# Performance work log

Measured on AMD Instinct MI355X. Metric: run time of the kernel, lower is better.

## Reference

```python
import jax, jax.numpy as jnp
import numpy as np

EPS = 1e-10
N_ITERS = 20
TEMP = 1.0


def sinkhorn(log_alpha, temp, n_iters):
    # incomplete Sinkhorn normalization over last two dims
    la = log_alpha / temp
    for _ in range(n_iters):
        la = la - jax.nn.logsumexp(la, axis=-2, keepdims=True)  # column norm
        la = la - jax.nn.logsumexp(la, axis=-1, keepdims=True)  # row norm
    return jnp.exp(la)


def setup_inputs() -> dict:
    key = jax.random.key(0)
    k1, k2, k3 = jax.random.split(key, 3)
    S, B, D, N = 4, 8, 1024, 1024  # samples, batch, feature rows, perm size
    x = jax.random.normal(k1, (B, D, N), dtype=jnp.float32)
    # kaiming_uniform_ default (a=sqrt(5)) -> bound = 1/sqrt(fan_in)
    bound = 1.0 / np.sqrt(N)
    log_alpha = jax.random.uniform(k2, (N, N), jnp.float32, -bound, bound)
    u = jax.random.uniform(k3, (S, B, N, N), jnp.float32)  # uniform draws for gumbel
    return {"x": x, "log_alpha": log_alpha, "u": u}


def reference(x, log_alpha, u):
    # gumbel noise: -log(eps - log(U + eps)) as in sample_gumbel
    gumbel = -jnp.log(EPS - jnp.log(u + EPS))
    log_alpha_noise = log_alpha + gumbel                  # (S,B,N,N)
    soft_perms = sinkhorn(log_alpha_noise, TEMP, N_ITERS)  # (S,B,N,N)
    # x.unsqueeze(0) @ soft_perms -> (S,B,D,N)
    return jnp.einsum('bdn,sbnm->sbdm', x, soft_perms)
```

## Files before the change

### kernel.cpp

```cpp
#include <hip/hip_runtime.h>

#define EPS 1e-10f
#define NITERS 20
#define NN (1024*1024)

typedef __attribute__((ext_vector_type(8))) short bf16x8;
typedef __attribute__((ext_vector_type(4))) float f32x4;

__device__ __forceinline__ unsigned short f2bf(float f) {
  unsigned int x = __builtin_bit_cast(unsigned int, f);
  x += 0x7fffu + ((x >> 16) & 1u);
  return (unsigned short)(x >> 16);
}
__device__ __forceinline__ float bf2f(short s) {
  return __builtin_bit_cast(float, ((unsigned int)(unsigned short)s) << 16);
}

__global__ __launch_bounds__(256) void gumbel_colpass(const float* __restrict__ u,
                                                      const float* __restrict__ la,
                                                      unsigned short* __restrict__ Kb,
                                                      float* __restrict__ pv) {
  int bx = blockIdx.x;
  int sb = bx >> 4, ch = bx & 15;
  int tid = threadIdx.x, l = tid & 63, w = tid >> 6;
  int r0 = ch << 6;
  const float* ub = u + (size_t)sb * NN;
  float colacc[16];
#pragma unroll
  for (int k = 0; k < 16; ++k) colacc[k] = 0.f;

#pragma unroll 1
  for (int p = 0; p < 16; ++p) {
    int row = r0 + (p << 2) + w;
    const float4* u4 = (const float4*)(ub + (size_t)row * 1024 + l * 16);
    const float4* la4 = (const float4*)(la + (size_t)row * 1024 + l * 16);
    float kf[16];
#pragma unroll
    for (int q = 0; q < 4; ++q) {
      float4 uv = u4[q];
      float4 lv = la4[q];
      kf[q*4+0] = expf(lv.x) / (EPS - logf(uv.x + EPS));
      kf[q*4+1] = expf(lv.y) / (EPS - logf(uv.y + EPS));
      kf[q*4+2] = expf(lv.z) / (EPS - logf(uv.z + EPS));
      kf[q*4+3] = expf(lv.w) / (EPS - logf(uv.w + EPS));
    }
    bf16x8 o0, o1;
#pragma unroll
    for (int j = 0; j < 8; ++j) {
      o0[j] = (short)f2bf(kf[j]);
      o1[j] = (short)f2bf(kf[8 + j]);
      colacc[j] += kf[j];
      colacc[8 + j] += kf[8 + j];
    }
    bf16x8* kp = (bf16x8*)(Kb + (size_t)sb * NN + (size_t)row * 1024 + l * 16);
    kp[0] = o0; kp[1] = o1;
  }

  __shared__ float cacc[4][1024];
#pragma unroll
  for (int k = 0; k < 16; ++k) cacc[w][l * 16 + k] = colacc[k];
  __syncthreads();
  float4 s0 = *(float4*)&cacc[0][tid * 4];
  float4 s1 = *(float4*)&cacc[1][tid * 4];
  float4 s2 = *(float4*)&cacc[2][tid * 4];
  float4 s3 = *(float4*)&cacc[3][tid * 4];
  float4 s;
  s.x = s0.x + s1.x + s2.x + s3.x; s.y = s0.y + s1.y + s2.y + s3.y;
  s.z = s0.z + s1.z + s2.z + s3.z; s.w = s0.w + s1.w + s2.w + s3.w;
  ((float4*)pv)[((sb << 4) + ch) * 256 + tid] = s;
}

__global__ __launch_bounds__(256) void sinkhorn_fused(const unsigned short* __restrict__ Kb,
                                                      const float* __restrict__ pv_in,
                                                      float* __restrict__ pv_out) {
  int bx = blockIdx.x;
  int sb = bx >> 4, ch = bx & 15;
  int tid = threadIdx.x, l = tid & 63, w = tid >> 6;
  int r0 = ch << 6;
  __shared__ float smem[4][1024];

  {
    const float4* p4 = (const float4*)pv_in + (sb << 12);
    float4 s = make_float4(0.f, 0.f, 0.f, 0.f);
#pragma unroll
    for (int c = 0; c < 16; ++c) {
      float4 a = p4[c * 256 + tid];
      s.x += a.x; s.y += a.y; s.z += a.z; s.w += a.w;
    }
    float4 v4;
    v4.x = 1.f / s.x; v4.y = 1.f / s.y; v4.z = 1.f / s.z; v4.w = 1.f / s.w;
    *(float4*)&smem[0][tid * 4] = v4;
  }
  __syncthreads();
  float vreg[16];
#pragma unroll
  for (int k = 0; k < 16; ++k) vreg[k] = smem[0][l * 16 + k];
  __syncthreads();

  const unsigned short* Ks = Kb + (size_t)sb * NN;
  float colacc[16];
#pragma unroll
  for (int k = 0; k < 16; ++k) colacc[k] = 0.f;

#pragma unroll 2
  for (int p = 0; p < 16; ++p) {
    int row = r0 + (p << 2) + w;
    const bf16x8* kp = (const bf16x8*)(Ks + (size_t)row * 1024 + l * 16);
    bf16x8 k0 = kp[0], k1 = kp[1];
    float kf[16];
#pragma unroll
    for (int j = 0; j < 8; ++j) { kf[j] = bf2f(k0[j]); kf[8 + j] = bf2f(k1[j]); }
    float dot = 0.f;
#pragma unroll
    for (int k = 0; k < 16; ++k) dot += kf[k] * vreg[k];
#pragma unroll
    for (int m = 1; m < 64; m <<= 1) dot += __shfl_xor(dot, m, 64);
    float ui = 1.0f / dot;
#pragma unroll
    for (int k = 0; k < 16; ++k) colacc[k] += kf[k] * ui;
  }

#pragma unroll
  for (int k = 0; k < 16; ++k) smem[w][l * 16 + k] = colacc[k];
  __syncthreads();
  float4 s0 = *(float4*)&smem[0][tid * 4];
  float4 s1 = *(float4*)&smem[1][tid * 4];
  float4 s2 = *(float4*)&smem[2][tid * 4];
  float4 s3 = *(float4*)&smem[3][tid * 4];
  float4 s;
  s.x = s0.x + s1.x + s2.x + s3.x; s.y = s0.y + s1.y + s2.y + s3.y;
  s.z = s0.z + s1.z + s2.z + s3.z; s.w = s0.w + s1.w + s2.w + s3.w;
  ((float4*)pv_out)[((sb << 4) + ch) * 256 + tid] = s;
}

__global__ __launch_bounds__(256) void rowpass_pt(const unsigned short* __restrict__ Kb,
                                                  const float* __restrict__ pv_in,
                                                  unsigned short* __restrict__ Pt) {
  int bx = blockIdx.x;
  int sb = bx >> 4, ch = bx & 15;
  int tid = threadIdx.x, l = tid & 63, w = tid >> 6;
  int r0 = ch << 6;
  __shared__ float v_lds[1024];
  __shared__ float u_lds[64];
  __shared__ unsigned short tile[64][66];

  {
    const float4* p4 = (const float4*)pv_in + (sb << 12);
    float4 s = make_float4(0.f, 0.f, 0.f, 0.f);
#pragma unroll
    for (int c = 0; c < 16; ++c) {
      float4 a = p4[c * 256 + tid];
      s.x += a.x; s.y += a.y; s.z += a.z; s.w += a.w;
    }
    float4 v4;
    v4.x = 1.f / s.x; v4.y = 1.f / s.y; v4.z = 1.f / s.z; v4.w = 1.f / s.w;
    *(float4*)&v_lds[tid * 4] = v4;
  }
  __syncthreads();
  float vreg[16];
#pragma unroll
  for (int k = 0; k < 16; ++k) vreg[k] = v_lds[l * 16 + k];

  const unsigned short* Ks = Kb + (size_t)sb * NN;
#pragma unroll 2
  for (int p = 0; p < 16; ++p) {
    int row = r0 + (p << 2) + w;
    const bf16x8* kp = (const bf16x8*)(Ks + (size_t)row * 1024 + l * 16);
    bf16x8 k0 = kp[0], k1 = kp[1];
    float dot = 0.f;
#pragma unroll
    for (int j = 0; j < 8; ++j) dot += bf2f(k0[j]) * vreg[j] + bf2f(k1[j]) * vreg[8 + j];
#pragma unroll
    for (int m = 1; m < 64; m <<= 1) dot += __shfl_xor(dot, m, 64);
    if (l == 0) u_lds[(p << 2) + w] = 1.0f / dot;
  }
  __syncthreads();

  unsigned short* Pb = Pt + (size_t)sb * NN;
  int c = tid & 63, r4 = tid >> 6;
  for (int mt = 0; mt < 16; ++mt) {
    int m0 = mt << 6;
#pragma unroll
    for (int p = 0; p < 16; ++p) {
      int rr = (p << 2) + r4;
      float val = bf2f((short)Ks[(size_t)(r0 + rr) * 1024 + m0 + c]) * u_lds[rr] * v_lds[m0 + c];
      tile[rr][c] = f2bf(val);
    }
    __syncthreads();
#pragma unroll
    for (int p = 0; p < 16; ++p) {
      int rr = (p << 2) + r4;
      Pb[(size_t)(m0 + rr) * 1024 + r0 + c] = tile[c][rr];
    }
    __syncthreads();
  }
}

__global__ __launch_bounds__(256) void cvt_x(const float4* __restrict__ x4,
                                             unsigned short* __restrict__ xb) {
  int gid = blockIdx.x * 256 + threadIdx.x;
  float4 v = x4[gid];
  ushort4 o;
  o.x = f2bf(v.x); o.y = f2bf(v.y); o.z = f2bf(v.z); o.w = f2bf(v.w);
  *(ushort4*)&xb[(size_t)gid * 4] = o;
}

__global__ __launch_bounds__(256) void gemm_bf16(const unsigned short* __restrict__ xb,
                                                 const unsigned short* __restrict__ Pt,
                                                 float* __restrict__ out) {
  int bid = blockIdx.x;
  int lid = (bid & 7) * 256 + (bid >> 3);
  int sb = lid >> 6;
  int tm = (lid >> 3) & 7;
  int tn = lid & 7;
  int b = sb & 7;
  const unsigned short* A = xb + (size_t)b * NN;
  const unsigned short* Bt = Pt + (size_t)sb * NN;
  float* C = out + (size_t)sb * NN;

  __shared__ unsigned short lA[128 * 32];
  __shared__ unsigned short lB[128 * 32];

  int tid = threadIdx.x;
  int lane = tid & 63;
  int w = tid >> 6;
  int wm = (w >> 1) << 6;
  int wn = (w & 1) << 6;

  f32x4 acc[4][4] = {};

  int lr = tid >> 2;
  int lk = (tid & 3) << 3;
  const unsigned short* gA0 = A + (size_t)(tm * 128 + lr) * 1024 + lk;
  const unsigned short* gB0 = Bt + (size_t)(tn * 128 + lr) * 1024 + lk;

  for (int k0 = 0; k0 < 1024; k0 += 32) {
    __builtin_amdgcn_global_load_lds((const __attribute__((address_space(1))) void*)(gA0 + k0),
                                     (__attribute__((address_space(3))) void*)&lA[tid * 8], 16, 0, 0);
    __builtin_amdgcn_global_load_lds((const __attribute__((address_space(1))) void*)(gA0 + 64 * 1024 + k0),
                                     (__attribute__((address_space(3))) void*)&lA[2048 + tid * 8], 16, 0, 0);
    __builtin_amdgcn_global_load_lds((const __attribute__((address_space(1))) void*)(gB0 + k0),
                                     (__attribute__((address_space(3))) void*)&lB[tid * 8], 16, 0, 0);
    __builtin_amdgcn_global_load_lds((const __attribute__((address_space(1))) void*)(gB0 + 64 * 1024 + k0),
                                     (__attribute__((address_space(3))) void*)&lB[2048 + tid * 8], 16, 0, 0);
    __syncthreads();

    int kg = (lane >> 4) << 3;
    int rr = lane & 15;
    bf16x8 af[4], bfr[4];
#pragma unroll
    for (int mt = 0; mt < 4; ++mt)
      af[mt] = *(const bf16x8*)&lA[(wm + mt * 16 + rr) * 32 + kg];
#pragma unroll
    for (int nt = 0; nt < 4; ++nt)
      bfr[nt] = *(const bf16x8*)&lB[(wn + nt * 16 + rr) * 32 + kg];
#pragma unroll
    for (int mt = 0; mt < 4; ++mt)
#pragma unroll
      for (int nt = 0; nt < 4; ++nt)
        acc[mt][nt] = __builtin_amdgcn_mfma_f32_16x16x32_bf16(af[mt], bfr[nt], acc[mt][nt], 0, 0, 0);
    __syncthreads();
  }

  int col0 = lane & 15;
  int row0 = (lane >> 4) << 2;
#pragma unroll
  for (int mt = 0; mt < 4; ++mt) {
#pragma unroll
    for (int nt = 0; nt < 4; ++nt) {
      int row = tm * 128 + wm + mt * 16 + row0;
      int col = tn * 128 + wn + nt * 16 + col0;
#pragma unroll
      for (int r = 0; r < 4; ++r)
        C[(size_t)(row + r) * 1024 + col] = acc[mt][nt][r];
    }
  }
}

extern "C" void kernel_launch(void* const* d_in, const int* in_sizes, int n_in,
                              void* d_out, int out_size, void* d_ws, size_t ws_size,
                              hipStream_t stream) {
  (void)in_sizes; (void)n_in; (void)out_size;
  const float* x  = (const float*)d_in[0];
  const float* la = (const float*)d_in[1];
  const float* u  = (const float*)d_in[2];
  float* out = (float*)d_out;

  char* ws = (char*)d_ws;
  unsigned short* Kb = (unsigned short*)(ws);
  unsigned short* Pt = (unsigned short*)(ws + 67108864);
  unsigned short* xb = (unsigned short*)(ws + 134217728);
  float* pvA         = (float*)(ws + 150994944);
  float* pvB         = (float*)(ws + 153092096);
  if (ws_size < 155189248) return;

  gumbel_colpass<<<512, 256, 0, stream>>>(u, la, Kb, pvA);
  cvt_x<<<8192, 256, 0, stream>>>((const float4*)x, xb);

  float* pin = pvA;
  float* pout = pvB;
  for (int t = 1; t <= NITERS - 1; ++t) {
    sinkhorn_fused<<<512, 256, 0, stream>>>(Kb, pin, pout);
    float* tmp = pin; pin = pout; pout = tmp;
  }
  rowpass_pt<<<512, 256, 0, stream>>>(Kb, pin, Pt);

  gemm_bf16<<<2048, 256, 0, stream>>>(xb, Pt, out);
}
```

Before: 482.6 us.

## Fuse Sinkhorn iterations into one cooperative kernel with per-matrix spin barriers

Replaces the gumbel pass, the nineteen per-iteration Sinkhorn launches and the final row pass with a single cooperative kernel of 256 blocks of 512 threads. Each block owns a row chunk of one matrix and synchronises with the other fifteen chunks of that matrix through an atomic counter barrier, processing two groups of sixteen matrices in sequence. This removes about twenty kernel launches and their boundaries, and keeps each block's K chunk hot in cache across iterations. The cost is spin-wait barriers, only 256 blocks in flight, and serialising two matrix groups, which may underuse the GPU.

```diff
diff --git a/kernel.cpp b/kernel.cpp
--- a/kernel.cpp
+++ b/kernel.cpp
@@ -16,183 +16,197 @@
   return __builtin_bit_cast(float, ((unsigned int)(unsigned short)s) << 16);
 }
 
-__global__ __launch_bounds__(256) void gumbel_colpass(const float* __restrict__ u,
-                                                      const float* __restrict__ la,
-                                                      unsigned short* __restrict__ Kb,
-                                                      float* __restrict__ pv) {
-  int bx = blockIdx.x;
-  int sb = bx >> 4, ch = bx & 15;
-  int tid = threadIdx.x, l = tid & 63, w = tid >> 6;
-  int r0 = ch << 6;
-  const float* ub = u + (size_t)sb * NN;
-  float colacc[16];
-#pragma unroll
-  for (int k = 0; k < 16; ++k) colacc[k] = 0.f;
-
-#pragma unroll 1
-  for (int p = 0; p < 16; ++p) {
-    int row = r0 + (p << 2) + w;
-    const float4* u4 = (const float4*)(ub + (size_t)row * 1024 + l * 16);
-    const float4* la4 = (const float4*)(la + (size_t)row * 1024 + l * 16);
-    float kf[16];
-#pragma unroll
-    for (int q = 0; q < 4; ++q) {
-      float4 uv = u4[q];
-      float4 lv = la4[q];
-      kf[q*4+0] = expf(lv.x) / (EPS - logf(uv.x + EPS));
-      kf[q*4+1] = expf(lv.y) / (EPS - logf(uv.y + EPS));
-      kf[q*4+2] = expf(lv.z) / (EPS - logf(uv.z + EPS));
-      kf[q*4+3] = expf(lv.w) / (EPS - logf(uv.w + EPS));
-    }
-    bf16x8 o0, o1;
-#pragma unroll
-    for (int j = 0; j < 8; ++j) {
-      o0[j] = (short)f2bf(kf[j]);
-      o1[j] = (short)f2bf(kf[8 + j]);
-      colacc[j] += kf[j];
-      colacc[8 + j] += kf[8 + j];
-    }
-    bf16x8* kp = (bf16x8*)(Kb + (size_t)sb * NN + (size_t)row * 1024 + l * 16);
-    kp[0] = o0; kp[1] = o1;
-  }
-
-  __shared__ float cacc[4][1024];
-#pragma unroll
-  for (int k = 0; k < 16; ++k) cacc[w][l * 16 + k] = colacc[k];
+__device__ __forceinline__ void mat_barrier(unsigned* c, unsigned target) {
   __syncthreads();
-  float4 s0 = *(float4*)&cacc[0][tid * 4];
-  float4 s1 = *(float4*)&cacc[1][tid * 4];
-  float4 s2 = *(float4*)&cacc[2][tid * 4];
-  float4 s3 = *(float4*)&cacc[3][tid * 4];
-  float4 s;
-  s.x = s0.x + s1.x + s2.x + s3.x; s.y = s0.y + s1.y + s2.y + s3.y;
-  s.z = s0.z + s1.z + s2.z + s3.z; s.w = s0.w + s1.w + s2.w + s3.w;
-  ((float4*)pv)[((sb << 4) + ch) * 256 + tid] = s;
-}
-
-__global__ __launch_bounds__(256) void sinkhorn_fused(const unsigned short* __restrict__ Kb,
-                                                      const float* __restrict__ pv_in,
-                                                      float* __restrict__ pv_out) {
-  int bx = blockIdx.x;
-  int sb = bx >> 4, ch = bx & 15;
-  int tid = threadIdx.x, l = tid & 63, w = tid >> 6;
-  int r0 = ch << 6;
-  __shared__ float smem[4][1024];
-
-  {
-    const float4* p4 = (const float4*)pv_in + (sb << 12);
-    float4 s = make_float4(0.f, 0.f, 0.f, 0.f);
-#pragma unroll
-    for (int c = 0; c < 16; ++c) {
-      float4 a = p4[c * 256 + tid];
-      s.x += a.x; s.y += a.y; s.z += a.z; s.w += a.w;
-    }
-    float4 v4;
-    v4.x = 1.f / s.x; v4.y = 1.f / s.y; v4.z = 1.f / s.z; v4.w = 1.f / s.w;
-    *(float4*)&smem[0][tid * 4] = v4;
+  if (threadIdx.x == 0) {
+    __threadfence();
+    atomicAdd(c, 1u);
+    while (__hip_atomic_load(c, __ATOMIC_RELAXED, __HIP_MEMORY_SCOPE_AGENT) < target) {
+      __builtin_amdgcn_s_sleep(1);
+    }
+    __threadfence();
   }
   __syncthreads();
-  float vreg[16];
-#pragma unroll
-  for (int k = 0; k < 16; ++k) vreg[k] = smem[0][l * 16 + k];
-  __syncthreads();
-
-  const unsigned short* Ks = Kb + (size_t)sb * NN;
-  float colacc[16];
-#pragma unroll
-  for (int k = 0; k < 16; ++k) colacc[k] = 0.f;
-
-#pragma unroll 2
-  for (int p = 0; p < 16; ++p) {
-    int row = r0 + (p << 2) + w;
-    const bf16x8* kp = (const bf16x8*)(Ks + (size_t)row * 1024 + l * 16);
-    bf16x8 k0 = kp[0], k1 = kp[1];
-    float kf[16];
-#pragma unroll
-    for (int j = 0; j < 8; ++j) { kf[j] = bf2f(k0[j]); kf[8 + j] = bf2f(k1[j]); }
-    float dot = 0.f;
-#pragma unroll
-    for (int k = 0; k < 16; ++k) dot += kf[k] * vreg[k];
-#pragma unroll
-    for (int m = 1; m < 64; m <<= 1) dot += __shfl_xor(dot, m, 64);
-    float ui = 1.0f / dot;
-#pragma unroll
-    for (int k = 0; k < 16; ++k) colacc[k] += kf[k] * ui;
-  }
-
-#pragma unroll
-  for (int k = 0; k < 16; ++k) smem[w][l * 16 + k] = colacc[k];
-  __syncthreads();
-  float4 s0 = *(float4*)&smem[0][tid * 4];
-  float4 s1 = *(float4*)&smem[1][tid * 4];
-  float4 s2 = *(float4*)&smem[2][tid * 4];
-  float4 s3 = *(float4*)&smem[3][tid * 4];
-  float4 s;
-  s.x = s0.x + s1.x + s2.x + s3.x; s.y = s0.y + s1.y + s2.y + s3.y;
-  s.z = s0.z + s1.z + s2.z + s3.z; s.w = s0.w + s1.w + s2.w + s3.w;
-  ((float4*)pv_out)[((sb << 4) + ch) * 256 + tid] = s;
-}
-
-__global__ __launch_bounds__(256) void rowpass_pt(const unsigned short* __restrict__ Kb,
-                                                  const float* __restrict__ pv_in,
-                                                  unsigned short* __restrict__ Pt) {
-  int bx = blockIdx.x;
-  int sb = bx >> 4, ch = bx & 15;
-  int tid = threadIdx.x, l = tid & 63, w = tid >> 6;
+}
+
+__global__ __launch_bounds__(512) void sinkhorn_coop(const float* __restrict__ u,
+                                                     const float* __restrict__ la,
+                                                     unsigned short* __restrict__ Kb,
+                                                     float* __restrict__ pvA,
+                                                     float* __restrict__ pvB,
+                                                     unsigned short* __restrict__ Pt,
+                                                     unsigned* __restrict__ cnt) {
+  int bid = blockIdx.x;
+  int tid = threadIdx.x;
+  int l = tid & 63, w = tid >> 6;
+  int mloc = bid & 15;
+  int ch = bid >> 4;
   int r0 = ch << 6;
+
+  __shared__ float smem[8][1024];
   __shared__ float v_lds[1024];
   __shared__ float u_lds[64];
   __shared__ unsigned short tile[64][66];
 
-  {
-    const float4* p4 = (const float4*)pv_in + (sb << 12);
-    float4 s = make_float4(0.f, 0.f, 0.f, 0.f);
-#pragma unroll
-    for (int c = 0; c < 16; ++c) {
-      float4 a = p4[c * 256 + tid];
-      s.x += a.x; s.y += a.y; s.z += a.z; s.w += a.w;
-    }
-    float4 v4;
-    v4.x = 1.f / s.x; v4.y = 1.f / s.y; v4.z = 1.f / s.z; v4.w = 1.f / s.w;
-    *(float4*)&v_lds[tid * 4] = v4;
-  }
-  __syncthreads();
-  float vreg[16];
-#pragma unroll
-  for (int k = 0; k < 16; ++k) vreg[k] = v_lds[l * 16 + k];
-
-  const unsigned short* Ks = Kb + (size_t)sb * NN;
+  for (int g = 0; g < 2; ++g) {
+    int mat = g * 16 + mloc;
+    const float* ub = u + (size_t)mat * NN;
+    unsigned short* Ks = Kb + (size_t)mat * NN;
+    float* pA = pvA + ((size_t)mat << 14);
+    float* pB = pvB + ((size_t)mat << 14);
+    unsigned* c = cnt + mat;
+
+    {
+      float colacc[16];
+#pragma unroll
+      for (int k2 = 0; k2 < 16; ++k2) colacc[k2] = 0.f;
+#pragma unroll 1
+      for (int p = 0; p < 8; ++p) {
+        int row = r0 + (p << 3) + w;
+        const f32x4* u4 = (const f32x4*)(ub + (size_t)row * 1024 + l * 16);
+        const f32x4* la4 = (const f32x4*)(la + (size_t)row * 1024 + l * 16);
+        float kf[16];
+#pragma unroll
+        for (int q = 0; q < 4; ++q) {
+          f32x4 uv = __builtin_nontemporal_load(u4 + q);
+          f32x4 lv = __builtin_nontemporal_load(la4 + q);
+#pragma unroll
+          for (int e = 0; e < 4; ++e)
+            kf[q * 4 + e] = expf(lv[e]) / (EPS - logf(uv[e] + EPS));
+        }
+        bf16x8 o0, o1;
+#pragma unroll
+        for (int j = 0; j < 8; ++j) {
+          o0[j] = (short)f2bf(kf[j]);
+          o1[j] = (short)f2bf(kf[8 + j]);
+          colacc[j] += kf[j];
+          colacc[8 + j] += kf[8 + j];
+        }
+        bf16x8* kp = (bf16x8*)(Ks + (size_t)row * 1024 + l * 16);
+        kp[0] = o0; kp[1] = o1;
+      }
+#pragma unroll
+      for (int k2 = 0; k2 < 16; ++k2) smem[w][l * 16 + k2] = colacc[k2];
+      __syncthreads();
+      if (tid < 256) {
+        float4 s = make_float4(0.f, 0.f, 0.f, 0.f);
+#pragma unroll
+        for (int ww = 0; ww < 8; ++ww) {
+          float4 a = *(float4*)&smem[ww][tid * 4];
+          s.x += a.x; s.y += a.y; s.z += a.z; s.w += a.w;
+        }
+        *(float4*)&pA[(ch << 10) + tid * 4] = s;
+      }
+      mat_barrier(c, 16u);
+    }
+
+    const float* pin = pA;
+    float* pout = pB;
+#pragma unroll 1
+    for (int t = 1; t < NITERS; ++t) {
+      {
+        const float2* p2 = (const float2*)pin;
+        float2 s = make_float2(0.f, 0.f);
+#pragma unroll
+        for (int cch = 0; cch < 16; ++cch) {
+          float2 a = p2[cch * 512 + tid];
+          s.x += a.x; s.y += a.y;
+        }
+        v_lds[2 * tid] = 1.f / s.x;
+        v_lds[2 * tid + 1] = 1.f / s.y;
+      }
+      __syncthreads();
+      float vreg[16];
+#pragma unroll
+      for (int k2 = 0; k2 < 16; ++k2) vreg[k2] = v_lds[l * 16 + k2];
+
+      float colacc[16];
+#pragma unroll
+      for (int k2 = 0; k2 < 16; ++k2) colacc[k2] = 0.f;
 #pragma unroll 2
-  for (int p = 0; p < 16; ++p) {
-    int row = r0 + (p << 2) + w;
-    const bf16x8* kp = (const bf16x8*)(Ks + (size_t)row * 1024 + l * 16);
-    bf16x8 k0 = kp[0], k1 = kp[1];
-    float dot = 0.f;
-#pragma unroll
-    for (int j = 0; j < 8; ++j) dot += bf2f(k0[j]) * vreg[j] + bf2f(k1[j]) * vreg[8 + j];
-#pragma unroll
-    for (int m = 1; m < 64; m <<= 1) dot += __shfl_xor(dot, m, 64);
-    if (l == 0) u_lds[(p << 2) + w] = 1.0f / dot;
-  }
-  __syncthreads();
-
-  unsigned short* Pb = Pt + (size_t)sb * NN;
-  int c = tid & 63, r4 = tid >> 6;
-  for (int mt = 0; mt < 16; ++mt) {
-    int m0 = mt << 6;
-#pragma unroll
-    for (int p = 0; p < 16; ++p) {
-      int rr = (p << 2) + r4;
-      float val = bf2f((short)Ks[(size_t)(r0 + rr) * 1024 + m0 + c]) * u_lds[rr] * v_lds[m0 + c];
-      tile[rr][c] = f2bf(val);
+      for (int p = 0; p < 8; ++p) {
+        int row = r0 + (p << 3) + w;
+        const bf16x8* kp = (const bf16x8*)(Ks + (size_t)row * 1024 + l * 16);
+        bf16x8 k0 = kp[0], k1 = kp[1];
+        float kf[16];
+#pragma unroll
+        for (int j = 0; j < 8; ++j) { kf[j] = bf2f(k0[j]); kf[8 + j] = bf2f(k1[j]); }
+        float dot = 0.f;
+#pragma unroll
+        for (int k2 = 0; k2 < 16; ++k2) dot += kf[k2] * vreg[k2];
+#pragma unroll
+        for (int m = 1; m < 64; m <<= 1) dot += __shfl_xor(dot, m, 64);
+        float ui = 1.0f / dot;
+#pragma unroll
+        for (int k2 = 0; k2 < 16; ++k2) colacc[k2] += kf[k2] * ui;
+      }
+#pragma unroll
+      for (int k2 = 0; k2 < 16; ++k2) smem[w][l * 16 + k2] = colacc[k2];
+      __syncthreads();
+      if (tid < 256) {
+        float4 s = make_float4(0.f, 0.f, 0.f, 0.f);
+#pragma unroll
+        for (int ww = 0; ww < 8; ++ww) {
+          float4 a = *(float4*)&smem[ww][tid * 4];
+          s.x += a.x; s.y += a.y; s.z += a.z; s.w += a.w;
+        }
+        *(float4*)&pout[(ch << 10) + tid * 4] = s;
+      }
+      mat_barrier(c, 16u * (unsigned)(t + 1));
+      const float* tp = pout; pout = (float*)pin; pin = tp;
+    }
+
+    {
+      const float2* p2 = (const float2*)pin;
+      float2 s = make_float2(0.f, 0.f);
+#pragma unroll
+      for (int cch = 0; cch < 16; ++cch) {
+        float2 a = p2[cch * 512 + tid];
+        s.x += a.x; s.y += a.y;
+      }
+      v_lds[2 * tid] = 1.f / s.x;
+      v_lds[2 * tid + 1] = 1.f / s.y;
     }
     __syncthreads();
-#pragma unroll
-    for (int p = 0; p < 16; ++p) {
-      int rr = (p << 2) + r4;
-      Pb[(size_t)(m0 + rr) * 1024 + r0 + c] = tile[c][rr];
+    {
+      float vreg[16];
+#pragma unroll
+      for (int k2 = 0; k2 < 16; ++k2) vreg[k2] = v_lds[l * 16 + k2];
+#pragma unroll 1
+      for (int p = 0; p < 8; ++p) {
+        int row = r0 + (p << 3) + w;
+        const bf16x8* kp = (const bf16x8*)(Ks + (size_t)row * 1024 + l * 16);
+        bf16x8 k0 = kp[0], k1 = kp[1];
+        float dot = 0.f;
+#pragma unroll
+        for (int j = 0; j < 8; ++j) dot += bf2f(k0[j]) * vreg[j] + bf2f(k1[j]) * vreg[8 + j];
+#pragma unroll
+        for (int m = 1; m < 64; m <<= 1) dot += __shfl_xor(dot, m, 64);
+        if (l == 0) u_lds[(p << 3) + w] = 1.0f / dot;
+      }
     }
     __syncthreads();
+    {
+      unsigned short* Pb = Pt + (size_t)mat * NN;
+      int cc = tid & 63, r8 = tid >> 6;
+#pragma unroll 1
+      for (int mt = 0; mt < 16; ++mt) {
+        int m0 = mt << 6;
+#pragma unroll
+        for (int p = 0; p < 8; ++p) {
+          int rr = (p << 3) + r8;
+          float val = bf2f((short)Ks[(size_t)(r0 + rr) * 1024 + m0 + cc]) * u_lds[rr] * v_lds[m0 + cc];
+          tile[rr][cc] = f2bf(val);
+        }
+        __syncthreads();
+#pragma unroll
+        for (int p = 0; p < 8; ++p) {
+          int rr = (p << 3) + r8;
+          Pb[(size_t)(m0 + rr) * 1024 + r0 + cc] = tile[cc][rr];
+        }
+        __syncthreads();
+      }
+    }
   }
 }
 
@@ -292,18 +306,16 @@
   unsigned short* xb = (unsigned short*)(ws + 134217728);
   float* pvA         = (float*)(ws + 150994944);
   float* pvB         = (float*)(ws + 153092096);
-  if (ws_size < 155189248) return;
-
-  gumbel_colpass<<<512, 256, 0, stream>>>(u, la, Kb, pvA);
+  unsigned* cnt      = (unsigned*)(ws + 155189248);
+  if (ws_size < 155189376) return;
+
+  hipMemsetAsync(cnt, 0, 128, stream);
   cvt_x<<<8192, 256, 0, stream>>>((const float4*)x, xb);
 
-  float* pin = pvA;
-  float* pout = pvB;
-  for (int t = 1; t <= NITERS - 1; ++t) {
-    sinkhorn_fused<<<512, 256, 0, stream>>>(Kb, pin, pout);
-    float* tmp = pin; pin = pout; pout = tmp;
-  }
-  rowpass_pt<<<512, 256, 0, stream>>>(Kb, pin, Pt);
+  void* args[] = {(void*)&u, (void*)&la, (void*)&Kb, (void*)&pvA,
+                  (void*)&pvB, (void*)&Pt, (void*)&cnt};
+  hipLaunchCooperativeKernel((void*)sinkhorn_coop, dim3(256), dim3(512),
+                             args, 0, stream);
 
   gemm_bf16<<<2048, 256, 0, stream>>>(xb, Pt, out);
 }
```

After: 1.338 ms. 177% more time.
